# Performance work log

Hardware: AMD Instinct MI355X
Metric: run time of the kernel (lower is better)

Reference implementation:

```python
import jax, jax.numpy as jnp
import numpy as np

B, IN_CH, D = 16, 128, 2048
MID = IN_CH  # k=1
BN_EPS = 1e-5


def conv1x1(x, W, b):
    # x: [B, C, D], W: [O, C], b: [O] -> [B, O, D]
    return jnp.einsum('oc,bcd->bod', W, x) + b[None, :, None]


def batchnorm1d(y, gamma, beta):
    # training-mode BN over (batch, length) per channel, biased variance (torch default)
    m = jnp.mean(y, axis=(0, 2), keepdims=True)
    v = jnp.var(y, axis=(0, 2), keepdims=True)
    yhat = (y - m) * jax.lax.rsqrt(v + BN_EPS)
    return yhat * gamma[None, :, None] + beta[None, :, None]


def setup_inputs() -> dict:
    key = jax.random.key(0)
    ks = jax.random.split(key, 8)
    he = np.sqrt(2.0 / IN_CH)
    return {
        'x': jax.random.normal(ks[0], (B, IN_CH, D), dtype=jnp.float32),
        'Wf': jax.random.normal(ks[1], (MID, IN_CH), dtype=jnp.float32) * he,
        'bf': jnp.zeros((MID,), jnp.float32),
        'gamma_f': jnp.ones((MID,), jnp.float32),
        'beta_f': jnp.zeros((MID,), jnp.float32),
        'Wg': jax.random.normal(ks[2], (MID, IN_CH), dtype=jnp.float32) * he,
        'bg': jnp.zeros((MID,), jnp.float32),
        'gamma_g': jnp.ones((MID,), jnp.float32),
        'beta_g': jnp.zeros((MID,), jnp.float32),
        'Wh': jax.random.normal(ks[3], (MID, IN_CH), dtype=jnp.float32) * he,
        'bh': jnp.zeros((MID,), jnp.float32),
        'Wv': jax.random.normal(ks[4], (IN_CH, MID), dtype=jnp.float32) * 0.02,
        'bv': jnp.zeros((IN_CH,), jnp.float32),
    }


def reference(x, Wf, bf, gamma_f, beta_f, Wg, bg, gamma_g, beta_g, Wh, bh, Wv, bv):
    f_x = jax.nn.relu(batchnorm1d(conv1x1(x, Wf, bf), gamma_f, beta_f))  # [B, MID, D]
    g_x = jax.nn.relu(batchnorm1d(conv1x1(x, Wg, bg), gamma_g, beta_g))  # [B, MID, D]
    h_x = conv1x1(x, Wh, bh)                                             # [B, MID, D]
    # z[b,d,e] = sum_c f[b,c,d] * g[b,c,e]
    z = jnp.einsum('bcd,bce->bde', f_x, g_x)
    attn = jax.nn.softmax(z * (MID ** -0.5), axis=-1)  # [B, D, D]
    # z2[b,c,d] = sum_e attn[b,d,e] * h[b,c,e]
    z2 = jnp.einsum('bde,bce->bcd', attn, h_x)
    out = conv1x1(z2, Wv, bv) + x
    return out
```

## Files before the change

### kernel.cpp

```cpp
#include <hip/hip_runtime.h>
#include <math.h>

#define D_LEN 2048
#define C_CH  128
#define NB    16

typedef __attribute__((ext_vector_type(8))) short bf16x8;
typedef __attribute__((ext_vector_type(4))) float f32x4;

__device__ __forceinline__ unsigned int f2bf(float x){
    unsigned int u = __float_as_uint(x);
    return (u + 0x7fffu + ((u >> 16) & 1u)) >> 16;
}
__device__ __forceinline__ unsigned int pack2(float a, float b){
    return f2bf(a) | (f2bf(b) << 16);
}
__device__ __forceinline__ float bfl(unsigned int u){ return __uint_as_float(u << 16); }
__device__ __forceinline__ float bfh(unsigned int u){ return __uint_as_float(u & 0xffff0000u); }

__device__ __forceinline__ void gl_lds16(const void* g, void* l) {
    __builtin_amdgcn_global_load_lds(
        (const __attribute__((address_space(1))) unsigned int*)g,
        (__attribute__((address_space(3))) unsigned int*)l, 16, 0, 0);
}

__global__ __launch_bounds__(256) void conv3_kernel(
    const float* __restrict__ x,
    const float* __restrict__ Wf, const float* __restrict__ Wg,
    const float* __restrict__ Wh, const float* __restrict__ bh,
    short* __restrict__ ft, short* __restrict__ gt, short* __restrict__ hh,
    float* __restrict__ part)
{
    __shared__ __align__(16) char smem[34816 + 16384];
    float* xs  = (float*)smem;
    short* fgT = (short*)smem;
    short* hT  = (short*)smem;
    short* xt  = (short*)(smem + 34816);

    const int t    = threadIdx.x;
    const int lane = t & 63;
    const int w    = t >> 6;
    const int l15  = lane & 15, lg = lane >> 4;
    const int dblk = blockIdx.x * 64;
    const int b    = blockIdx.y;
    const int z    = blockIdx.z;
    const int bid  = b * 32 + blockIdx.x;
    const size_t xbase = (size_t)b * C_CH * D_LEN;
    const float* W = (z == 0) ? Wf : (z == 1) ? Wg : Wh;

    #pragma unroll
    for (int k = 0; k < 8; ++k) {
        int u = t + k * 256;
        int c = u >> 4, d4 = (u & 15) * 4;
        float4 v = *(const float4*)(x + xbase + (size_t)c * D_LEN + dblk + d4);
        *(float4*)&xs[c * 68 + d4] = v;
    }
    __syncthreads();

    {
        const int d  = t & 63;
        const int cw = t >> 6;
        #pragma unroll
        for (int k = 0; k < 4; ++k) {
            int c0 = (cw + 4 * k) * 8;
            float v[8];
            #pragma unroll
            for (int j = 0; j < 8; ++j) v[j] = xs[(c0 + j) * 68 + d];
            uint4 o;
            o.x = pack2(v[0], v[1]); o.y = pack2(v[2], v[3]);
            o.z = pack2(v[4], v[5]); o.w = pack2(v[6], v[7]);
            *(uint4*)&xt[d * 128 + (c0 ^ ((d & 7) << 3))] = o;
        }
    }
    __syncthreads();

    const f32x4 fzero = {0.f, 0.f, 0.f, 0.f};

    bf16x8 af[2][4];
    #pragma unroll
    for (int ot = 0; ot < 2; ++ot) {
        int o = (w * 2 + ot) * 16 + l15;
        #pragma unroll
        for (int ks = 0; ks < 4; ++ks) {
            const float* wp = W + o * 128 + ks * 32 + lg * 8;
            float4 v0 = *(const float4*)wp;
            float4 v1 = *(const float4*)(wp + 4);
            uint4 pk;
            pk.x = pack2(v0.x, v0.y); pk.y = pack2(v0.z, v0.w);
            pk.z = pack2(v1.x, v1.y); pk.w = pack2(v1.z, v1.w);
            af[ot][ks] = *(bf16x8*)&pk;
        }
    }

    f32x4 acc[2][4];
    #pragma unroll
    for (int ot = 0; ot < 2; ++ot)
        #pragma unroll
        for (int dg = 0; dg < 4; ++dg) acc[ot][dg] = fzero;

    #pragma unroll
    for (int dg = 0; dg < 4; ++dg) {
        int d = dg * 16 + l15;
        #pragma unroll
        for (int ks = 0; ks < 4; ++ks) {
            bf16x8 bx = *(const bf16x8*)&xt[d * 128 + ((ks * 32 + lg * 8) ^ ((d & 7) << 3))];
            acc[0][dg] = __builtin_amdgcn_mfma_f32_16x16x32_bf16(af[0][ks], bx, acc[0][dg], 0, 0, 0);
            acc[1][dg] = __builtin_amdgcn_mfma_f32_16x16x32_bf16(af[1][ks], bx, acc[1][dg], 0, 0, 0);
        }
    }

    if (z < 2) {
        float* ps  = part + (size_t)(z * 2 + 0) * 65536;
        float* pss = part + (size_t)(z * 2 + 1) * 65536;
        #pragma unroll
        for (int ot = 0; ot < 2; ++ot) {
            #pragma unroll
            for (int r = 0; r < 4; ++r) {
                float a0 = acc[ot][0][r], a1 = acc[ot][1][r];
                float a2 = acc[ot][2][r], a3 = acc[ot][3][r];
                float s = (a0 + a1) + (a2 + a3);
                float q = (a0 * a0 + a1 * a1) + (a2 * a2 + a3 * a3);
                s += __shfl_xor(s, 1); s += __shfl_xor(s, 2);
                s += __shfl_xor(s, 4); s += __shfl_xor(s, 8);
                q += __shfl_xor(q, 1); q += __shfl_xor(q, 2);
                q += __shfl_xor(q, 4); q += __shfl_xor(q, 8);
                if (l15 == 0) {
                    int o = (w * 2 + ot) * 16 + lg * 4 + r;
                    ps [o * 512 + bid] = s;
                    pss[o * 512 + bid] = q;
                }
            }
        }
        #pragma unroll
        for (int ot = 0; ot < 2; ++ot) {
            #pragma unroll
            for (int dg = 0; dg < 4; ++dg) {
                int row = dg * 16 + l15;
                int col = (w * 2 + ot) * 16 + lg * 4;
                uint2 p;
                p.x = pack2(acc[ot][dg][0], acc[ot][dg][1]);
                p.y = pack2(acc[ot][dg][2], acc[ot][dg][3]);
                *(uint2*)&fgT[row * 128 + (col ^ ((row & 7) << 3))] = p;
            }
        }
        __syncthreads();
        short* Y = z ? gt : ft;
        #pragma unroll
        for (int k = 0; k < 4; ++k) {
            int u = t + k * 256;
            int row = u >> 4, c8 = (u & 15) * 8;
            uint4 v = *(const uint4*)&fgT[row * 128 + (c8 ^ ((row & 7) << 3))];
            *(uint4*)&Y[((size_t)b * D_LEN + dblk + row) * C_CH + c8] = v;
        }
    } else {
        #pragma unroll
        for (int ot = 0; ot < 2; ++ot) {
            #pragma unroll
            for (int r = 0; r < 4; ++r) {
                int o = (w * 2 + ot) * 16 + lg * 4 + r;
                float bo = bh[o];
                #pragma unroll
                for (int dg = 0; dg < 4; ++dg)
                    hT[o * 72 + dg * 16 + l15] = (short)f2bf(acc[ot][dg][r] + bo);
            }
        }
        __syncthreads();
        #pragma unroll
        for (int k = 0; k < 4; ++k) {
            int idx = t + k * 256;
            int row = idx >> 3, q8 = (idx & 7) * 8;
            uint4 v = *(const uint4*)&hT[row * 72 + q8];
            *(uint4*)&hh[((size_t)(b * C_CH) + row) * D_LEN + dblk + q8] = v;
        }
    }
}

__global__ __launch_bounds__(256) void bnstat2_kernel(
    const float* __restrict__ part,
    const float* __restrict__ gf, const float* __restrict__ btf,
    const float* __restrict__ gg, const float* __restrict__ btg,
    float* __restrict__ coefA, float* __restrict__ coefB)
{
    const int ch = blockIdx.x;
    const int which = ch >> 7, c = ch & 127;
    const int t = threadIdx.x;
    const float* ps  = part + (size_t)(which * 2 + 0) * 65536 + c * 512;
    const float* pss = part + (size_t)(which * 2 + 1) * 65536 + c * 512;
    float2 sv = *(const float2*)&ps[t * 2];
    float2 qv = *(const float2*)&pss[t * 2];
    float s = sv.x + sv.y, q = qv.x + qv.y;
    #pragma unroll
    for (int off = 32; off > 0; off >>= 1) {
        s += __shfl_xor(s, off);
        q += __shfl_xor(q, off);
    }
    __shared__ float rs[4], rq[4];
    if ((t & 63) == 0) { rs[t >> 6] = s; rq[t >> 6] = q; }
    __syncthreads();
    if (t == 0) {
        s = rs[0] + rs[1] + rs[2] + rs[3];
        q = rq[0] + rq[1] + rq[2] + rq[3];
        const float inv = 1.0f / 32768.0f;
        const float SQ  = 0.29730177875068026f * 1.2011224087864498f;
        float m    = s * inv;
        float var  = q * inv - m * m;
        float rstd = rsqrtf(var + 1e-5f);
        float gma  = which ? gg[c] : gf[c];
        float bta  = which ? btg[c] : btf[c];
        float a    = gma * rstd;
        coefA[ch] = a * SQ;
        coefB[ch] = (bta - m * a) * SQ;
    }
}

__global__ __launch_bounds__(256) void bnapply_kernel(
    short* __restrict__ ft, short* __restrict__ gt,
    const float* __restrict__ coefA, const float* __restrict__ coefB)
{
    const int gid   = blockIdx.x * 256 + threadIdx.x;
    const int which = gid >> 19;
    const int idx   = gid & 524287;
    short* Y = which ? gt : ft;
    const int c0 = (idx & 15) * 8;
    const float4 a0 = *(const float4*)&coefA[which * 128 + c0];
    const float4 a1 = *(const float4*)&coefA[which * 128 + c0 + 4];
    const float4 b0 = *(const float4*)&coefB[which * 128 + c0];
    const float4 b1 = *(const float4*)&coefB[which * 128 + c0 + 4];
    uint4 v = *(const uint4*)&Y[(size_t)idx * 8];
    uint4 o;
    o.x = pack2(fmaxf(fmaf(a0.x, bfl(v.x), b0.x), 0.f),
                fmaxf(fmaf(a0.y, bfh(v.x), b0.y), 0.f));
    o.y = pack2(fmaxf(fmaf(a0.z, bfl(v.y), b0.z), 0.f),
                fmaxf(fmaf(a0.w, bfh(v.y), b0.w), 0.f));
    o.z = pack2(fmaxf(fmaf(a1.x, bfl(v.z), b1.x), 0.f),
                fmaxf(fmaf(a1.y, bfh(v.z), b1.y), 0.f));
    o.w = pack2(fmaxf(fmaf(a1.z, bfl(v.w), b1.z), 0.f),
                fmaxf(fmaf(a1.w, bfh(v.w), b1.w), 0.f));
    *(uint4*)&Y[(size_t)idx * 8] = o;
}

#define M_SHIFT2 8.656170245333781f

__global__ __launch_bounds__(256) void flashattn_kernel(
    const short* __restrict__ ft, const short* __restrict__ gt,
    const short* __restrict__ hh, short* __restrict__ z2t)
{
    __shared__ __align__(16) short g_lds[2][64 * 128];
    __shared__ __align__(16) short h_lds[2][128 * 64];
    __shared__ __align__(16) short p_lds[64 * 64];

    const int t    = threadIdx.x;
    const int lane = t & 63;
    const int w    = t >> 6;
    const int l15  = lane & 15, lg = lane >> 4;

    const int L  = blockIdx.x;
    const int r_ = L >> 3;
    const int b    = (L & 7) * 2 + (r_ >> 5);
    const int dblk = (r_ & 31) * 64;

    const size_t gbase = (size_t)b * D_LEN * C_CH;
    const size_t hbase = (size_t)(b * C_CH) * D_LEN;

    const int g_row  = t >> 4;
    const int g_colS = (t & 15) * 8;
    const int h_row  = t >> 3;
    const int h_colS = (t & 7) * 8;

    auto stage_issue = [&](int e0, int bb) {
        #pragma unroll
        for (int k = 0; k < 4; ++k) {
            int row = g_row + k * 16;
            const short* src = gt + gbase + (size_t)(e0 + row) * C_CH
                             + (g_colS ^ ((row & 7) << 3));
            gl_lds16(src, &g_lds[bb][k * 2048 + t * 8]);
        }
        #pragma unroll
        for (int k = 0; k < 4; ++k) {
            int row = h_row + k * 32;
            const short* src = hh + hbase + (size_t)row * D_LEN + e0
                             + (h_colS ^ ((row & 7) << 3));
            gl_lds16(src, &h_lds[bb][k * 2048 + t * 8]);
        }
    };

    {
        const size_t fb = gbase + (size_t)dblk * C_CH;
        #pragma unroll
        for (int k = 0; k < 4; ++k) {
            int row = g_row + k * 16;
            uint4 v = *(const uint4*)(ft + fb + (size_t)row * C_CH + g_colS);
            *(uint4*)&g_lds[0][(row * 128 + g_colS) ^ ((row & 7) << 3)] = v;
        }
    }
    __syncthreads();
    const int drow = w * 16 + l15;
    bf16x8 bfrag[4];
    #pragma unroll
    for (int ks = 0; ks < 4; ++ks)
        bfrag[ks] = *(const bf16x8*)&g_lds[0][(drow * 128 + ks * 32 + lg * 8) ^ ((drow & 7) << 3)];
    __syncthreads();

    stage_issue(0, 0);
    stage_issue(64, 1);

    float l_run = 0.f;
    const f32x4 fzero = {0.f, 0.f, 0.f, 0.f};
    f32x4 acc[8];
    #pragma unroll
    for (int n = 0; n < 8; ++n) acc[n] = fzero;

    for (int i = 0; i < 32; ++i) {
        const int cur = i & 1;
        const short* gl = g_lds[cur];
        const short* hl = h_lds[cur];

        if (i < 31) asm volatile("s_waitcnt vmcnt(8)" ::: "memory");
        else        asm volatile("s_waitcnt vmcnt(0)" ::: "memory");
        __builtin_amdgcn_s_barrier();

        f32x4 st[4];
        #pragma unroll
        for (int m = 0; m < 4; ++m) st[m] = fzero;
        __builtin_amdgcn_s_setprio(1);
        #pragma unroll
        for (int m = 0; m < 4; ++m) {
            int erow = m * 16 + l15;
            #pragma unroll
            for (int ks = 0; ks < 4; ++ks) {
                bf16x8 ag = *(const bf16x8*)&gl[(erow * 128 + ks * 32 + lg * 8) ^ ((erow & 7) << 3)];
                st[m] = __builtin_amdgcn_mfma_f32_16x16x32_bf16(ag, bfrag[ks], st[m], 0, 0, 0);
            }
        }
        __builtin_amdgcn_s_setprio(0);

        float psum = 0.f;
        #pragma unroll
        for (int m = 0; m < 4; ++m) {
            float p0 = exp2f(st[m][0] - M_SHIFT2);
            float p1 = exp2f(st[m][1] - M_SHIFT2);
            float p2 = exp2f(st[m][2] - M_SHIFT2);
            float p3 = exp2f(st[m][3] - M_SHIFT2);
            psum += (p0 + p1) + (p2 + p3);
            uint2 pv;
            pv.x = pack2(p0, p1);
            pv.y = pack2(p2, p3);
            *(uint2*)&p_lds[(drow * 64 + m * 16 + lg * 4) ^ ((drow & 7) << 3)] = pv;
        }
        psum += __shfl_xor(psum, 16);
        psum += __shfl_xor(psum, 32);
        l_run += psum;

        asm volatile("s_waitcnt lgkmcnt(0)" ::: "memory");
        __builtin_amdgcn_sched_barrier(0);

        bf16x8 pa[2];
        #pragma unroll
        for (int ks = 0; ks < 2; ++ks)
            pa[ks] = *(const bf16x8*)&p_lds[(drow * 64 + ks * 32 + lg * 8) ^ ((drow & 7) << 3)];
        __builtin_amdgcn_s_setprio(1);
        #pragma unroll
        for (int n = 0; n < 8; ++n) {
            int crow = n * 16 + l15;
            #pragma unroll
            for (int ks = 0; ks < 2; ++ks) {
                bf16x8 hb_ = *(const bf16x8*)&hl[(crow * 64 + ks * 32 + lg * 8) ^ ((crow & 7) << 3)];
                acc[n] = __builtin_amdgcn_mfma_f32_16x16x32_bf16(pa[ks], hb_, acc[n], 0, 0, 0);
            }
        }
        __builtin_amdgcn_s_setprio(0);

        __builtin_amdgcn_s_barrier();
        if (i + 2 < 32) stage_issue((i + 2) * 64, cur);
    }

    float rl[4];
    #pragma unroll
    for (int r = 0; r < 4; ++r)
        rl[r] = 1.0f / __shfl(l_run, lg * 4 + r);

    __syncthreads();
    #pragma unroll
    for (int n = 0; n < 8; ++n) {
        int col = n * 16 + l15;
        #pragma unroll
        for (int r = 0; r < 4; ++r) {
            int row = w * 16 + lg * 4 + r;
            g_lds[0][row * 128 + (col ^ ((row & 7) << 3))] = (short)f2bf(acc[n][r] * rl[r]);
        }
    }
    __syncthreads();
    {
        const size_t zb = ((size_t)b * D_LEN + dblk) * C_CH;
        #pragma unroll
        for (int k = 0; k < 4; ++k) {
            int u = t + k * 256;
            int row = u >> 4, c8 = (u & 15) * 8;
            uint4 v = *(const uint4*)&g_lds[0][row * 128 + (c8 ^ ((row & 7) << 3))];
            *(uint4*)&z2t[zb + (size_t)row * C_CH + c8] = v;
        }
    }
}

__global__ __launch_bounds__(256) void convout_kernel(
    const short* __restrict__ z2t, const float* __restrict__ Wv,
    const float* __restrict__ bv, const float* __restrict__ x,
    float* __restrict__ out)
{
    __shared__ __align__(16) short zt[64 * 128];

    const int t    = threadIdx.x;
    const int lane = t & 63;
    const int w    = t >> 6;
    const int l15  = lane & 15, lg = lane >> 4;
    const int dblk = blockIdx.x * 64;
    const int b    = blockIdx.y;
    const size_t base = (size_t)b * C_CH * D_LEN;

    {
        const size_t zb = ((size_t)b * D_LEN + dblk) * C_CH;
        #pragma unroll
        for (int k = 0; k < 4; ++k) {
            int u = t + k * 256;
            int row = u >> 4, cq = (u & 15) * 8;
            uint4 v = *(const uint4*)(z2t + zb + (size_t)row * C_CH + cq);
            *(uint4*)&zt[(row * 128 + cq) ^ ((row & 7) << 3)] = v;
        }
    }

    bf16x8 af[2][4];
    #pragma unroll
    for (int ot = 0; ot < 2; ++ot) {
        int o = (w * 2 + ot) * 16 + l15;
        #pragma unroll
        for (int ks = 0; ks < 4; ++ks) {
            const float* wp = Wv + o * 128 + ks * 32 + lg * 8;
            float4 v0 = *(const float4*)wp;
            float4 v1 = *(const float4*)(wp + 4);
            uint4 pk;
            pk.x = pack2(v0.x, v0.y); pk.y = pack2(v0.z, v0.w);
            pk.z = pack2(v1.x, v1.y); pk.w = pack2(v1.z, v1.w);
            af[ot][ks] = *(bf16x8*)&pk;
        }
    }
    __syncthreads();

    const f32x4 fzero = {0.f, 0.f, 0.f, 0.f};
    f32x4 acc[2][4];
    #pragma unroll
    for (int ot = 0; ot < 2; ++ot)
        #pragma unroll
        for (int dg = 0; dg < 4; ++dg) acc[ot][dg] = fzero;

    #pragma unroll
    for (int dg = 0; dg < 4; ++dg) {
        int d = dg * 16 + l15;
        #pragma unroll
        for (int ks = 0; ks < 4; ++ks) {
            bf16x8 bx = *(const bf16x8*)&zt[d * 128 + ((ks * 32 + lg * 8) ^ ((d & 7) << 3))];
            acc[0][dg] = __builtin_amdgcn_mfma_f32_16x16x32_bf16(af[0][ks], bx, acc[0][dg], 0, 0, 0);
            acc[1][dg] = __builtin_amdgcn_mfma_f32_16x16x32_bf16(af[1][ks], bx, acc[1][dg], 0, 0, 0);
        }
    }

    #pragma unroll
    for (int ot = 0; ot < 2; ++ot) {
        #pragma unroll
        for (int r = 0; r < 4; ++r) {
            int o = (w * 2 + ot) * 16 + lg * 4 + r;
            float bo = bv[o];
            const float* xr  = x   + base + (size_t)o * D_LEN + dblk;
            float*      orow = out + base + (size_t)o * D_LEN + dblk;
            #pragma unroll
            for (int dg = 0; dg < 4; ++dg) {
                int d = dg * 16 + l15;
                orow[d] = acc[ot][dg][r] + bo + xr[d];
            }
        }
    }
}

extern "C" void kernel_launch(void* const* d_in, const int* in_sizes, int n_in,
                              void* d_out, int out_size, void* d_ws, size_t ws_size,
                              hipStream_t stream)
{
    const float* x   = (const float*)d_in[0];
    const float* Wf  = (const float*)d_in[1];
    const float* gf  = (const float*)d_in[3];
    const float* btf = (const float*)d_in[4];
    const float* Wg  = (const float*)d_in[5];
    const float* gg  = (const float*)d_in[7];
    const float* btg = (const float*)d_in[8];
    const float* Wh  = (const float*)d_in[9];
    const float* bh  = (const float*)d_in[10];
    const float* Wv  = (const float*)d_in[11];
    const float* bv  = (const float*)d_in[12];
    float* out = (float*)d_out;

    const size_t elems = (size_t)NB * C_CH * D_LEN;
    short* ft    = (short*)d_ws;
    short* gt    = ft + elems;
    short* hh    = gt + elems;
    short* z2t   = hh + elems;
    float* part  = (float*)(z2t + elems);
    float* coefA = part + 262144;
    float* coefB = coefA + 256;

    conv3_kernel<<<dim3(32, NB, 3), 256, 0, stream>>>(
        x, Wf, Wg, Wh, bh, ft, gt, hh, part);
    bnstat2_kernel<<<dim3(256), 256, 0, stream>>>(
        part, gf, btf, gg, btg, coefA, coefB);
    bnapply_kernel<<<dim3(4096), 256, 0, stream>>>(ft, gt, coefA, coefB);
    flashattn_kernel<<<dim3(512), 256, 0, stream>>>(ft, gt, hh, z2t);
    convout_kernel<<<dim3(32, NB), 256, 0, stream>>>(z2t, Wv, bv, x, out);
}
```

Before: 186.4 us.

## Fuse output conv into flash-attention epilogue and use native exp/bf16 convert

The output 1x1 conv plus bias and residual is moved into the flash-attention kernel's epilogue. The normalized z2 tile now stays in LDS instead of going through a global z2t buffer and a separate launch. The softmax shift is folded into the MFMA accumulator init, and exp2 plus bf16 packing use raw v_exp_f32 and v_cvt_pk_bf16_f32 instructions instead of exp2f and software rounding. This removes one kernel launch and a global round trip of z2. The attention kernel's epilogue grows, which adds register pressure and makes it longer.

```diff
diff --git a/kernel.cpp b/kernel.cpp
--- a/kernel.cpp
+++ b/kernel.cpp
@@ -17,6 +17,13 @@
 }
 __device__ __forceinline__ float bfl(unsigned int u){ return __uint_as_float(u << 16); }
 __device__ __forceinline__ float bfh(unsigned int u){ return __uint_as_float(u & 0xffff0000u); }
+
+__device__ __forceinline__ float exp2v(float x){
+    float r; asm("v_exp_f32 %0, %1" : "=v"(r) : "v"(x)); return r;
+}
+__device__ __forceinline__ unsigned int cvtpk(float a, float b){
+    unsigned int r; asm("v_cvt_pk_bf16_f32 %0, %1, %2" : "=v"(r) : "v"(a), "v"(b)); return r;
+}
 
 __device__ __forceinline__ void gl_lds16(const void* g, void* l) {
     __builtin_amdgcn_global_load_lds(
@@ -228,13 +235,13 @@
     const float4 b1 = *(const float4*)&coefB[which * 128 + c0 + 4];
     uint4 v = *(const uint4*)&Y[(size_t)idx * 8];
     uint4 o;
-    o.x = pack2(fmaxf(fmaf(a0.x, bfl(v.x), b0.x), 0.f),
+    o.x = cvtpk(fmaxf(fmaf(a0.x, bfl(v.x), b0.x), 0.f),
                 fmaxf(fmaf(a0.y, bfh(v.x), b0.y), 0.f));
-    o.y = pack2(fmaxf(fmaf(a0.z, bfl(v.y), b0.z), 0.f),
+    o.y = cvtpk(fmaxf(fmaf(a0.z, bfl(v.y), b0.z), 0.f),
                 fmaxf(fmaf(a0.w, bfh(v.y), b0.w), 0.f));
-    o.z = pack2(fmaxf(fmaf(a1.x, bfl(v.z), b1.x), 0.f),
+    o.z = cvtpk(fmaxf(fmaf(a1.x, bfl(v.z), b1.x), 0.f),
                 fmaxf(fmaf(a1.y, bfh(v.z), b1.y), 0.f));
-    o.w = pack2(fmaxf(fmaf(a1.z, bfl(v.w), b1.z), 0.f),
+    o.w = cvtpk(fmaxf(fmaf(a1.z, bfl(v.w), b1.z), 0.f),
                 fmaxf(fmaf(a1.w, bfh(v.w), b1.w), 0.f));
     *(uint4*)&Y[(size_t)idx * 8] = o;
 }
@@ -243,7 +250,9 @@
 
 __global__ __launch_bounds__(256) void flashattn_kernel(
     const short* __restrict__ ft, const short* __restrict__ gt,
-    const short* __restrict__ hh, short* __restrict__ z2t)
+    const short* __restrict__ hh, const float* __restrict__ Wv,
+    const float* __restrict__ bv, const float* __restrict__ x,
+    float* __restrict__ out)
 {
     __shared__ __align__(16) short g_lds[2][64 * 128];
     __shared__ __align__(16) short h_lds[2][128 * 64];
@@ -306,6 +315,7 @@
 
     float l_run = 0.f;
     const f32x4 fzero = {0.f, 0.f, 0.f, 0.f};
+    const f32x4 minit = {-M_SHIFT2, -M_SHIFT2, -M_SHIFT2, -M_SHIFT2};
     f32x4 acc[8];
     #pragma unroll
     for (int n = 0; n < 8; ++n) acc[n] = fzero;
@@ -321,7 +331,7 @@
 
         f32x4 st[4];
         #pragma unroll
-        for (int m = 0; m < 4; ++m) st[m] = fzero;
+        for (int m = 0; m < 4; ++m) st[m] = minit;
         __builtin_amdgcn_s_setprio(1);
         #pragma unroll
         for (int m = 0; m < 4; ++m) {
@@ -337,14 +347,14 @@
         float psum = 0.f;
         #pragma unroll
         for (int m = 0; m < 4; ++m) {
-            float p0 = exp2f(st[m][0] - M_SHIFT2);
-            float p1 = exp2f(st[m][1] - M_SHIFT2);
-            float p2 = exp2f(st[m][2] - M_SHIFT2);
-            float p3 = exp2f(st[m][3] - M_SHIFT2);
+            float p0 = exp2v(st[m][0]);
+            float p1 = exp2v(st[m][1]);
+            float p2 = exp2v(st[m][2]);
+            float p3 = exp2v(st[m][3]);
             psum += (p0 + p1) + (p2 + p3);
             uint2 pv;
-            pv.x = pack2(p0, p1);
-            pv.y = pack2(p2, p3);
+            pv.x = cvtpk(p0, p1);
+            pv.y = cvtpk(p2, p3);
             *(uint2*)&p_lds[(drow * 64 + m * 16 + lg * 4) ^ ((drow & 7) << 3)] = pv;
         }
         psum += __shfl_xor(psum, 16);
@@ -379,6 +389,7 @@
     for (int r = 0; r < 4; ++r)
         rl[r] = 1.0f / __shfl(l_run, lg * 4 + r);
 
+    short* gl0 = &g_lds[0][0];
     __syncthreads();
     #pragma unroll
     for (int n = 0; n < 8; ++n) {
@@ -386,45 +397,7 @@
         #pragma unroll
         for (int r = 0; r < 4; ++r) {
             int row = w * 16 + lg * 4 + r;
-            g_lds[0][row * 128 + (col ^ ((row & 7) << 3))] = (short)f2bf(acc[n][r] * rl[r]);
-        }
-    }
-    __syncthreads();
-    {
-        const size_t zb = ((size_t)b * D_LEN + dblk) * C_CH;
-        #pragma unroll
-        for (int k = 0; k < 4; ++k) {
-            int u = t + k * 256;
-            int row = u >> 4, c8 = (u & 15) * 8;
-            uint4 v = *(const uint4*)&g_lds[0][row * 128 + (c8 ^ ((row & 7) << 3))];
-            *(uint4*)&z2t[zb + (size_t)row * C_CH + c8] = v;
-        }
-    }
-}
-
-__global__ __launch_bounds__(256) void convout_kernel(
-    const short* __restrict__ z2t, const float* __restrict__ Wv,
-    const float* __restrict__ bv, const float* __restrict__ x,
-    float* __restrict__ out)
-{
-    __shared__ __align__(16) short zt[64 * 128];
-
-    const int t    = threadIdx.x;
-    const int lane = t & 63;
-    const int w    = t >> 6;
-    const int l15  = lane & 15, lg = lane >> 4;
-    const int dblk = blockIdx.x * 64;
-    const int b    = blockIdx.y;
-    const size_t base = (size_t)b * C_CH * D_LEN;
-
-    {
-        const size_t zb = ((size_t)b * D_LEN + dblk) * C_CH;
-        #pragma unroll
-        for (int k = 0; k < 4; ++k) {
-            int u = t + k * 256;
-            int row = u >> 4, cq = (u & 15) * 8;
-            uint4 v = *(const uint4*)(z2t + zb + (size_t)row * C_CH + cq);
-            *(uint4*)&zt[(row * 128 + cq) ^ ((row & 7) << 3)] = v;
+            gl0[row * 128 + (col ^ ((row & 7) << 3))] = (short)f2bf(acc[n][r] * rl[r]);
         }
     }
 
@@ -445,24 +418,24 @@
     }
     __syncthreads();
 
-    const f32x4 fzero = {0.f, 0.f, 0.f, 0.f};
-    f32x4 acc[2][4];
+    f32x4 acc2[2][4];
     #pragma unroll
     for (int ot = 0; ot < 2; ++ot)
         #pragma unroll
-        for (int dg = 0; dg < 4; ++dg) acc[ot][dg] = fzero;
+        for (int dg = 0; dg < 4; ++dg) acc2[ot][dg] = fzero;
 
     #pragma unroll
     for (int dg = 0; dg < 4; ++dg) {
         int d = dg * 16 + l15;
         #pragma unroll
         for (int ks = 0; ks < 4; ++ks) {
-            bf16x8 bx = *(const bf16x8*)&zt[d * 128 + ((ks * 32 + lg * 8) ^ ((d & 7) << 3))];
-            acc[0][dg] = __builtin_amdgcn_mfma_f32_16x16x32_bf16(af[0][ks], bx, acc[0][dg], 0, 0, 0);
-            acc[1][dg] = __builtin_amdgcn_mfma_f32_16x16x32_bf16(af[1][ks], bx, acc[1][dg], 0, 0, 0);
-        }
-    }
-
+            bf16x8 bx = *(const bf16x8*)&gl0[d * 128 + ((ks * 32 + lg * 8) ^ ((d & 7) << 3))];
+            acc2[0][dg] = __builtin_amdgcn_mfma_f32_16x16x32_bf16(af[0][ks], bx, acc2[0][dg], 0, 0, 0);
+            acc2[1][dg] = __builtin_amdgcn_mfma_f32_16x16x32_bf16(af[1][ks], bx, acc2[1][dg], 0, 0, 0);
+        }
+    }
+
+    const size_t base = (size_t)b * C_CH * D_LEN;
     #pragma unroll
     for (int ot = 0; ot < 2; ++ot) {
         #pragma unroll
@@ -474,7 +447,7 @@
             #pragma unroll
             for (int dg = 0; dg < 4; ++dg) {
                 int d = dg * 16 + l15;
-                orow[d] = acc[ot][dg][r] + bo + xr[d];
+                orow[d] = acc2[ot][dg][r] + bo + xr[d];
             }
         }
     }
@@ -501,8 +474,7 @@
     short* ft    = (short*)d_ws;
     short* gt    = ft + elems;
     short* hh    = gt + elems;
-    short* z2t   = hh + elems;
-    float* part  = (float*)(z2t + elems);
+    float* part  = (float*)(hh + elems);
     float* coefA = part + 262144;
     float* coefB = coefA + 256;
 
@@ -511,6 +483,6 @@
     bnstat2_kernel<<<dim3(256), 256, 0, stream>>>(
         part, gf, btf, gg, btg, coefA, coefB);
     bnapply_kernel<<<dim3(4096), 256, 0, stream>>>(ft, gt, coefA, coefB);
-    flashattn_kernel<<<dim3(512), 256, 0, stream>>>(ft, gt, hh, z2t);
-    convout_kernel<<<dim3(32, NB), 256, 0, stream>>>(z2t, Wv, bv, x, out);
-}
+    flashattn_kernel<<<dim3(512), 256, 0, stream>>>(
+        ft, gt, hh, Wv, bv, x, out);
+}
```

Result: faster. 177.7 us (-4.7%).
